# Performance work log

Hardware: AMD Instinct MI355X
Metric: run time of the kernel (lower is better)

## Reference

```python
import jax, jax.numpy as jnp
import numpy as np

H = 128  # lstm_hidden_dim


def setup_inputs() -> dict:
    key = jax.random.key(0)
    ks = jax.random.split(key, 7)
    T, B, D = 512, 1024, 128
    s = 1.0 / np.sqrt(H)  # pytorch default LSTM init scale
    return {
        "inp": jax.random.normal(ks[0], (T, B, D), dtype=jnp.float32),
        "W_ih": jax.random.uniform(ks[1], (4 * H, D), jnp.float32, -s, s),
        "W_hh": jax.random.uniform(ks[2], (4 * H, H), jnp.float32, -s, s),
        "b_ih": jax.random.uniform(ks[3], (4 * H,), jnp.float32, -s, s),
        "b_hh": jax.random.uniform(ks[4], (4 * H,), jnp.float32, -s, s),
        "W_lin": jax.random.uniform(ks[5], (H, H), jnp.float32, -s, s),
        "b_lin": jax.random.uniform(ks[6], (H,), jnp.float32, -s, s),
        "future": 128,
    }


def _lstm_cell(x, h, c, W_ih, W_hh, b_ih, b_hh):
    # gates: [B, 4H], PyTorch gate order i, f, g, o
    gates = x @ W_ih.T + b_ih + h @ W_hh.T + b_hh
    i, f, g, o = jnp.split(gates, 4, axis=-1)
    i, f, o = jax.nn.sigmoid(i), jax.nn.sigmoid(f), jax.nn.sigmoid(o)
    g = jnp.tanh(g)
    c_new = f * c + i * g
    h_new = o * jnp.tanh(c_new)
    return h_new, c_new


def reference(inp, W_ih, W_hh, b_ih, b_hh, W_lin, b_lin, future):
    B = inp.shape[1]
    h0 = jnp.zeros((B, H), inp.dtype)
    c0 = jnp.zeros((B, H), inp.dtype)

    def scan_step(carry, x):
        h, c = carry
        h, c = _lstm_cell(x, h, c, W_ih, W_hh, b_ih, b_hh)
        return (h, c), None

    (h, c), _ = jax.lax.scan(scan_step, (h0, c0), inp)
    out = h @ W_lin.T + b_lin  # [B, H]

    def fut_step(carry, _):
        o, h, c = carry
        h, c = _lstm_cell(o, h, c, W_ih, W_hh, b_ih, b_hh)
        o = h @ W_lin.T + b_lin
        return (o, h, c), o

    (_, _, _), fut_outs = jax.lax.scan(fut_step, (out, h, c), None, length=future)
    # outputs: [future + 1, B, H]
    return jnp.concatenate([out[None], fut_outs], axis=0)
```

## Files before the change

### kernel.cpp

```cpp
#include <hip/hip_runtime.h>

#define TSTEPS 512
#define BATCH  1024
#define DIM    128
#define HID    128
#define FUT    128
#define BTILE  4
#define NBLOCKS (BATCH / BTILE)
#define NTHREADS 512
#define LSTR   136

typedef __bf16 bf16x8 __attribute__((ext_vector_type(8)));
typedef float  f32x4  __attribute__((ext_vector_type(4)));
typedef unsigned int uint32x2 __attribute__((ext_vector_type(2)));

#define LOG2E 1.4426950408889634f

#if defined(__has_builtin)
#if __has_builtin(__builtin_amdgcn_permlane16_swap) && __has_builtin(__builtin_amdgcn_permlane32_swap)
#define HAVE_PERMSWAP 1
#endif
#endif
#ifndef HAVE_PERMSWAP
#define HAVE_PERMSWAP 0
#endif

__device__ __forceinline__ bf16x8 ldfrag(const float* __restrict__ p) {
    f32x4 a = *(const f32x4*)p;
    f32x4 b = *(const f32x4*)(p + 4);
    bf16x8 r;
    r[0] = (__bf16)a[0]; r[1] = (__bf16)a[1]; r[2] = (__bf16)a[2]; r[3] = (__bf16)a[3];
    r[4] = (__bf16)b[0]; r[5] = (__bf16)b[1]; r[6] = (__bf16)b[2]; r[7] = (__bf16)b[3];
    return r;
}

__device__ __forceinline__ float cell_update(f32x4 gv, float& c) {
    float pi = gv[0], pf = gv[1], pg = gv[2], po = gv[3];
    float ti = __builtin_amdgcn_exp2f(-LOG2E        * __builtin_fabsf(pi));
    float tf = __builtin_amdgcn_exp2f(-LOG2E        * __builtin_fabsf(pf));
    float tg = __builtin_amdgcn_exp2f(-2.0f * LOG2E * __builtin_fabsf(pg));
    float to = __builtin_amdgcn_exp2f(-LOG2E        * __builtin_fabsf(po));
    float di = 1.0f + ti, df = 1.0f + tf, dg = 1.0f + tg, dox = 1.0f + to;
    float p1 = di * df, p2 = dg * dox;
    float invP  = __builtin_amdgcn_rcpf(p1 * p2);
    float inv12 = invP * p2;
    float inv34 = invP * p1;
    float ig = ((pi >= 0.0f) ? 1.0f : ti) * (inv12 * df);
    float fg = ((pf >= 0.0f) ? 1.0f : tf) * (inv12 * di);
    float og = ((po >= 0.0f) ? 1.0f : to) * (inv34 * dg);
    float gg = __builtin_copysignf((1.0f - tg) * (inv34 * dox), pg);
    c = fg * c + ig * gg;
    float tc  = __builtin_amdgcn_exp2f(-2.0f * LOG2E * __builtin_fabsf(c));
    float thc = __builtin_copysignf((1.0f - tc) * __builtin_amdgcn_rcpf(1.0f + tc), c);
    return og * thc;
}

__device__ __forceinline__ float sel4(int q, float b0, float b1, float b2, float b3) {
    float lo = (q & 1) ? b1 : b0;
    float hi = (q & 1) ? b3 : b2;
    return (q & 2) ? hi : lo;
}

#if HAVE_PERMSWAP
__device__ __forceinline__ float gate_gather_perm(f32x4 a, bool r1_16, bool r1_32) {
    uint32x2 s01 = __builtin_amdgcn_permlane16_swap(__float_as_uint(a[0]), __float_as_uint(a[1]), false, false);
    uint32x2 s23 = __builtin_amdgcn_permlane16_swap(__float_as_uint(a[2]), __float_as_uint(a[3]), false, false);
    unsigned lo = r1_16 ? s01[1] : s01[0];
    unsigned hi = r1_16 ? s23[1] : s23[0];
    uint32x2 fin = __builtin_amdgcn_permlane32_swap(lo, hi, false, false);
    return __uint_as_float(r1_32 ? fin[1] : fin[0]);
}
#endif

__global__ __launch_bounds__(NTHREADS, 2)
void lstm_forecast(const float* __restrict__ inp,
                   const float* __restrict__ W_ih, const float* __restrict__ W_hh,
                   const float* __restrict__ b_ih, const float* __restrict__ b_hh,
                   const float* __restrict__ W_lin, const float* __restrict__ b_lin,
                   float* __restrict__ out)
{
    __shared__ __bf16 x_sh[2][16 * LSTR];
    __shared__ __bf16 h_sh[2][16 * LSTR];

    const int tid  = threadIdx.x;
    const int lane = tid & 63;
    const int wave = tid >> 6;
    const int q    = lane >> 4;
    const int m    = lane & 15;
    const int bo   = blockIdx.x * BTILE;

    for (int i = tid; i < 16 * LSTR; i += NTHREADS) {
        x_sh[0][i] = (__bf16)0.0f;
        x_sh[1][i] = (__bf16)0.0f;
        h_sh[0][i] = (__bf16)0.0f;
        h_sh[1][i] = (__bf16)0.0f;
    }

    bool use_perm = false, r1_16 = false, r1_32 = false;
    int  fmap = 0;
#if HAVE_PERMSWAP
    {
        unsigned lid = (unsigned)lane;
        uint32x2 t16 = __builtin_amdgcn_permlane16_swap(lid, lid + 1000u, false, false);
        unsigned v16 = (unsigned)__builtin_amdgcn_readlane((int)t16[0], 0);
        uint32x2 t32 = __builtin_amdgcn_permlane32_swap(lid, lid + 1000u, false, false);
        unsigned v32 = (unsigned)__builtin_amdgcn_readlane((int)t32[0], 0);
        bool ok16 = (v16 == 0u) || (v16 == 16u) || (v16 == 1000u) || (v16 == 1016u);
        bool ok32 = (v32 == 0u) || (v32 == 32u) || (v32 == 1000u) || (v32 == 1032u);
        r1_16 = (v16 == 16u) || (v16 == 1016u);
        r1_32 = (v32 == 32u) || (v32 == 1032u);
        bool fl16 = (v16 >= 1000u);
        bool fl32 = (v32 >= 1000u);
        use_perm = ok16 && ok32;
        fmap = (fl16 ? 1 : 0) | (fl32 ? 2 : 0);
    }
#endif

    bf16x8 wih[4][4], whh[4][4], wlin[4];
    float  bias_g[4];
    #pragma unroll
    for (int g = 0; g < 4; ++g) {
        const int n = g * HID + wave * 16 + m;
        bias_g[g] = b_ih[n] + b_hh[n];
        #pragma unroll
        for (int kt = 0; kt < 4; ++kt) {
            wih[g][kt] = ldfrag(W_ih + (size_t)n * DIM + kt * 32 + q * 8);
            whh[g][kt] = ldfrag(W_hh + (size_t)n * HID + kt * 32 + q * 8);
        }
    }
    const int   nl     = wave * 16 + m;
    const float bias_l = b_lin[nl];
    #pragma unroll
    for (int kt = 0; kt < 4; ++kt)
        wlin[kt] = ldfrag(W_lin + (size_t)nl * HID + kt * 32 + q * 8);

    const int rb = use_perm ? (q ^ fmap) : q;
    const int jj = wave * 16 + m;
    float creg = 0.0f;

    const int lk    = m * LSTR + q * 8;
    const int paddr = (lane & 15) << 2;

    const int cr = tid >> 7, cc = tid & 127;
    const float* xptr = inp + (size_t)(bo + cr) * DIM + cc;
    const size_t XS = (size_t)BATCH * DIM;
    const int xrowb = 4 * (use_perm ? (cr ^ fmap) : cr);

    float bank0[8], bank1[8];
    #pragma unroll
    for (int k = 0; k < 8; ++k) {
        bank0[k] = xptr[(size_t)k * XS];
        bank1[k] = xptr[(size_t)(8 + k) * XS];
    }

    __syncthreads();

    f32x4 xacc[4];

    for (int tb = 0; tb < TSTEPS; tb += 16) {
        #pragma unroll
        for (int j = 0; j < 16; ++j) {
            const int p = j & 1;
            if ((j & 3) == 0) {
                #pragma unroll
                for (int k = 0; k < 4; ++k) {
                    float xv = ((j + k) < 8) ? bank0[j + k] : bank1[j + k - 8];
                    x_sh[0][(xrowb + k) * LSTR + cc] = (__bf16)xv;
                }
            }
            __syncthreads();

            if (j == 7) {
                if (tb + 16 < TSTEPS) {
                    #pragma unroll
                    for (int k = 0; k < 8; ++k)
                        bank0[k] = xptr[(size_t)(tb + 16 + k) * XS];
                }
            }
            if (j == 15) {
                if (tb + 24 < TSTEPS) {
                    #pragma unroll
                    for (int k = 0; k < 8; ++k)
                        bank1[k] = xptr[(size_t)(tb + 24 + k) * XS];
                }
            }

            if ((j & 3) == 0) {
                #pragma unroll
                for (int g = 0; g < 4; ++g)
                    xacc[g] = (f32x4){bias_g[g], bias_g[g], bias_g[g], bias_g[g]};
                #pragma unroll
                for (int kt = 0; kt < 4; ++kt) {
                    bf16x8 ax = *(const bf16x8*)&x_sh[0][lk + kt * 32];
                    #pragma unroll
                    for (int g = 0; g < 4; ++g)
                        xacc[g] = __builtin_amdgcn_mfma_f32_16x16x32_bf16(ax, wih[g][kt], xacc[g], 0, 0, 0);
                }
            }

            f32x4 hacc[4];
            #pragma unroll
            for (int g = 0; g < 4; ++g)
                hacc[g] = (f32x4){0.0f, 0.0f, 0.0f, 0.0f};
            #pragma unroll
            for (int kt = 0; kt < 4; ++kt) {
                bf16x8 ah = *(const bf16x8*)&h_sh[p][lk + kt * 32];
                #pragma unroll
                for (int g = 0; g < 4; ++g)
                    hacc[g] = __builtin_amdgcn_mfma_f32_16x16x32_bf16(ah, whh[g][kt], hacc[g], 0, 0, 0);
            }

            f32x4 gv;
#if HAVE_PERMSWAP
            if (use_perm) {
                #pragma unroll
                for (int g = 0; g < 4; ++g)
                    gv[g] = gate_gather_perm(hacc[g], r1_16, r1_32) + xacc[g][j & 3];
            } else
#endif
            {
                #pragma unroll
                for (int g = 0; g < 4; ++g) {
                    float b0 = __int_as_float(__builtin_amdgcn_ds_bpermute(paddr, __float_as_int(hacc[g][0])));
                    float b1 = __int_as_float(__builtin_amdgcn_ds_bpermute(paddr, __float_as_int(hacc[g][1])));
                    float b2 = __int_as_float(__builtin_amdgcn_ds_bpermute(paddr, __float_as_int(hacc[g][2])));
                    float b3 = __int_as_float(__builtin_amdgcn_ds_bpermute(paddr, __float_as_int(hacc[g][3])));
                    gv[g] = sel4(q, b0, b1, b2, b3) + xacc[g][j & 3];
                }
            }

            float h = cell_update(gv, creg);
            h_sh[p ^ 1][rb * LSTR + jj] = (__bf16)h;
        }
    }

    for (int i = tid; i < 16 * LSTR; i += NTHREADS)
        if (i >= 4 * LSTR) x_sh[0][i] = (__bf16)0.0f;

    int ph = 0;
    for (int tf = 0; tf <= FUT; ++tf) {
        __syncthreads();
        f32x4 accl = (f32x4){bias_l, bias_l, bias_l, bias_l};
        #pragma unroll
        for (int kt = 0; kt < 4; ++kt) {
            bf16x8 ah = *(const bf16x8*)&h_sh[ph][lk + kt * 32];
            accl = __builtin_amdgcn_mfma_f32_16x16x32_bf16(ah, wlin[kt], accl, 0, 0, 0);
        }
        if (q == 0) {
            #pragma unroll
            for (int r = 0; r < 4; ++r) {
                float o = accl[r];
                out[(size_t)tf * BATCH * HID + (size_t)(bo + r) * HID + nl] = o;
                if (tf < FUT) {
                    __bf16 hi = (__bf16)o;
                    x_sh[0][r * LSTR + nl] = hi;
                    x_sh[1][r * LSTR + nl] = (__bf16)(o - (float)hi);
                }
            }
        }
        if (tf == FUT) break;
        __syncthreads();

        f32x4 acc[4];
        #pragma unroll
        for (int g = 0; g < 4; ++g)
            acc[g] = (f32x4){bias_g[g], bias_g[g], bias_g[g], bias_g[g]};
        #pragma unroll
        for (int kt = 0; kt < 4; ++kt) {
            bf16x8 axh = *(const bf16x8*)&x_sh[0][lk + kt * 32];
            bf16x8 axl = *(const bf16x8*)&x_sh[1][lk + kt * 32];
            bf16x8 ah  = *(const bf16x8*)&h_sh[ph][lk + kt * 32];
            #pragma unroll
            for (int g = 0; g < 4; ++g) {
                acc[g] = __builtin_amdgcn_mfma_f32_16x16x32_bf16(axh, wih[g][kt], acc[g], 0, 0, 0);
                acc[g] = __builtin_amdgcn_mfma_f32_16x16x32_bf16(axl, wih[g][kt], acc[g], 0, 0, 0);
                acc[g] = __builtin_amdgcn_mfma_f32_16x16x32_bf16(ah,  whh[g][kt], acc[g], 0, 0, 0);
            }
        }
        f32x4 gv;
#if HAVE_PERMSWAP
        if (use_perm) {
            #pragma unroll
            for (int g = 0; g < 4; ++g)
                gv[g] = gate_gather_perm(acc[g], r1_16, r1_32);
        } else
#endif
        {
            #pragma unroll
            for (int g = 0; g < 4; ++g) {
                float b0 = __int_as_float(__builtin_amdgcn_ds_bpermute(paddr, __float_as_int(acc[g][0])));
                float b1 = __int_as_float(__builtin_amdgcn_ds_bpermute(paddr, __float_as_int(acc[g][1])));
                float b2 = __int_as_float(__builtin_amdgcn_ds_bpermute(paddr, __float_as_int(acc[g][2])));
                float b3 = __int_as_float(__builtin_amdgcn_ds_bpermute(paddr, __float_as_int(acc[g][3])));
                gv[g] = sel4(q, b0, b1, b2, b3);
            }
        }

        float h = cell_update(gv, creg);
        h_sh[ph ^ 1][rb * LSTR + jj] = (__bf16)h;
        ph ^= 1;
    }
}

extern "C" void kernel_launch(void* const* d_in, const int* in_sizes, int n_in,
                              void* d_out, int out_size, void* d_ws, size_t ws_size,
                              hipStream_t stream) {
    const float* inp   = (const float*)d_in[0];
    const float* W_ih  = (const float*)d_in[1];
    const float* W_hh  = (const float*)d_in[2];
    const float* b_ih  = (const float*)d_in[3];
    const float* b_hh  = (const float*)d_in[4];
    const float* W_lin = (const float*)d_in[5];
    const float* b_lin = (const float*)d_in[6];
    float* out = (float*)d_out;

    hipLaunchKernelGGL(lstm_forecast, dim3(NBLOCKS), dim3(NTHREADS), 0, stream,
                       inp, W_ih, W_hh, b_ih, b_hh, W_lin, b_lin, out);
}
```

Measured before the change: 845.3 us.

## Fold linear projection into future-step LSTM weights via precomputed fused matrix

Adds a prep kernel that computes W_fut = W_hh + W_ih·W_lin and a fused bias (b_ih + b_hh + W_ih·b_lin), so each future step needs one 128-wide matmul on h instead of separate x (hi/lo split) and h matmuls plus an extra barrier. It also masks h fragment loads to the 4 valid batch rows so LDS reads for padding rows are skipped. The fused weight is rounded to bf16, which drops the hi/lo precision split on the output feedback and may add error over 128 recurrent steps. It also costs one extra kernel launch and a global weight read per block.

```diff
diff --git a/kernel.cpp b/kernel.cpp
--- a/kernel.cpp
+++ b/kernel.cpp
@@ -25,12 +25,22 @@
 #define HAVE_PERMSWAP 0
 #endif
 
+__device__ __bf16 g_wfut[4 * HID * HID];
+__device__ float  g_wfutb[4 * HID];
+
 __device__ __forceinline__ bf16x8 ldfrag(const float* __restrict__ p) {
     f32x4 a = *(const f32x4*)p;
     f32x4 b = *(const f32x4*)(p + 4);
     bf16x8 r;
     r[0] = (__bf16)a[0]; r[1] = (__bf16)a[1]; r[2] = (__bf16)a[2]; r[3] = (__bf16)a[3];
     r[4] = (__bf16)b[0]; r[5] = (__bf16)b[1]; r[6] = (__bf16)b[2]; r[7] = (__bf16)b[3];
+    return r;
+}
+
+__device__ __forceinline__ bf16x8 zfrag() {
+    bf16x8 r;
+    #pragma unroll
+    for (int i = 0; i < 8; ++i) r[i] = (__bf16)0.0f;
     return r;
 }
 
@@ -72,6 +82,39 @@
 }
 #endif
 
+__global__ __launch_bounds__(512)
+void prep_wfut(const float* __restrict__ W_ih, const float* __restrict__ W_hh,
+               const float* __restrict__ b_ih, const float* __restrict__ b_hh,
+               const float* __restrict__ W_lin, const float* __restrict__ b_lin)
+{
+    __shared__ float wl[64 * 128];
+    __shared__ float sc[512];
+    const int tid = threadIdx.x;
+    const int r = tid >> 7, k = tid & 127;
+    const int n = blockIdx.x * 4 + r;
+
+    float acc = W_hh[(size_t)n * HID + k];
+    #pragma unroll
+    for (int half = 0; half < 2; ++half) {
+        __syncthreads();
+        for (int i = tid; i < 64 * 128; i += 512)
+            wl[i] = W_lin[half * 64 * 128 + i];
+        __syncthreads();
+        #pragma unroll 8
+        for (int d = 0; d < 64; ++d)
+            acc += W_ih[(size_t)n * DIM + half * 64 + d] * wl[d * 128 + k];
+    }
+    g_wfut[(size_t)n * HID + k] = (__bf16)acc;
+
+    sc[tid] = W_ih[(size_t)n * DIM + k] * b_lin[k];
+    __syncthreads();
+    for (int s = 64; s > 0; s >>= 1) {
+        if (k < s) sc[r * 128 + k] += sc[r * 128 + k + s];
+        __syncthreads();
+    }
+    if (k == 0) g_wfutb[n] = b_ih[n] + b_hh[n] + sc[r * 128];
+}
+
 __global__ __launch_bounds__(NTHREADS, 2)
 void lstm_forecast(const float* __restrict__ inp,
                    const float* __restrict__ W_ih, const float* __restrict__ W_hh,
@@ -79,7 +122,7 @@
                    const float* __restrict__ W_lin, const float* __restrict__ b_lin,
                    float* __restrict__ out)
 {
-    __shared__ __bf16 x_sh[2][16 * LSTR];
+    __shared__ __bf16 x_sh[16 * LSTR];
     __shared__ __bf16 h_sh[2][16 * LSTR];
 
     const int tid  = threadIdx.x;
@@ -90,8 +133,7 @@
     const int bo   = blockIdx.x * BTILE;
 
     for (int i = tid; i < 16 * LSTR; i += NTHREADS) {
-        x_sh[0][i] = (__bf16)0.0f;
-        x_sh[1][i] = (__bf16)0.0f;
+        x_sh[i] = (__bf16)0.0f;
         h_sh[0][i] = (__bf16)0.0f;
         h_sh[1][i] = (__bf16)0.0f;
     }
@@ -165,7 +207,7 @@
                 #pragma unroll
                 for (int k = 0; k < 4; ++k) {
                     float xv = ((j + k) < 8) ? bank0[j + k] : bank1[j + k - 8];
-                    x_sh[0][(xrowb + k) * LSTR + cc] = (__bf16)xv;
+                    x_sh[(xrowb + k) * LSTR + cc] = (__bf16)xv;
                 }
             }
             __syncthreads();
@@ -191,7 +233,7 @@
                     xacc[g] = (f32x4){bias_g[g], bias_g[g], bias_g[g], bias_g[g]};
                 #pragma unroll
                 for (int kt = 0; kt < 4; ++kt) {
-                    bf16x8 ax = *(const bf16x8*)&x_sh[0][lk + kt * 32];
+                    bf16x8 ax = *(const bf16x8*)&x_sh[lk + kt * 32];
                     #pragma unroll
                     for (int g = 0; g < 4; ++g)
                         xacc[g] = __builtin_amdgcn_mfma_f32_16x16x32_bf16(ax, wih[g][kt], xacc[g], 0, 0, 0);
@@ -204,7 +246,8 @@
                 hacc[g] = (f32x4){0.0f, 0.0f, 0.0f, 0.0f};
             #pragma unroll
             for (int kt = 0; kt < 4; ++kt) {
-                bf16x8 ah = *(const bf16x8*)&h_sh[p][lk + kt * 32];
+                bf16x8 ah = zfrag();
+                if (m < BTILE) ah = *(const bf16x8*)&h_sh[p][lk + kt * 32];
                 #pragma unroll
                 for (int g = 0; g < 4; ++g)
                     hacc[g] = __builtin_amdgcn_mfma_f32_16x16x32_bf16(ah, whh[g][kt], hacc[g], 0, 0, 0);
@@ -234,64 +277,64 @@
         }
     }
 
-    for (int i = tid; i < 16 * LSTR; i += NTHREADS)
-        if (i >= 4 * LSTR) x_sh[0][i] = (__bf16)0.0f;
+    bf16x8 wfut[4][4];
+    float  bias_f[4];
+    #pragma unroll
+    for (int g = 0; g < 4; ++g) {
+        const int n = g * HID + nl;
+        bias_f[g] = g_wfutb[n];
+        #pragma unroll
+        for (int kt = 0; kt < 4; ++kt)
+            wfut[g][kt] = *(const bf16x8*)(g_wfut + (size_t)n * HID + kt * 32 + q * 8);
+    }
 
     int ph = 0;
     for (int tf = 0; tf <= FUT; ++tf) {
         __syncthreads();
+        bf16x8 ahf[4];
+        #pragma unroll
+        for (int kt = 0; kt < 4; ++kt) {
+            ahf[kt] = zfrag();
+            if (m < BTILE) ahf[kt] = *(const bf16x8*)&h_sh[ph][lk + kt * 32];
+        }
+
         f32x4 accl = (f32x4){bias_l, bias_l, bias_l, bias_l};
         #pragma unroll
+        for (int kt = 0; kt < 4; ++kt)
+            accl = __builtin_amdgcn_mfma_f32_16x16x32_bf16(ahf[kt], wlin[kt], accl, 0, 0, 0);
+        if (q == 0) {
+            #pragma unroll
+            for (int r = 0; r < 4; ++r)
+                out[(size_t)tf * BATCH * HID + (size_t)(bo + r) * HID + nl] = accl[r];
+        }
+        if (tf == FUT) break;
+
+        f32x4 facc[4];
+        #pragma unroll
+        for (int g = 0; g < 4; ++g)
+            facc[g] = (f32x4){bias_f[g], bias_f[g], bias_f[g], bias_f[g]};
+        #pragma unroll
         for (int kt = 0; kt < 4; ++kt) {
-            bf16x8 ah = *(const bf16x8*)&h_sh[ph][lk + kt * 32];
-            accl = __builtin_amdgcn_mfma_f32_16x16x32_bf16(ah, wlin[kt], accl, 0, 0, 0);
-        }
-        if (q == 0) {
-            #pragma unroll
-            for (int r = 0; r < 4; ++r) {
-                float o = accl[r];
-                out[(size_t)tf * BATCH * HID + (size_t)(bo + r) * HID + nl] = o;
-                if (tf < FUT) {
-                    __bf16 hi = (__bf16)o;
-                    x_sh[0][r * LSTR + nl] = hi;
-                    x_sh[1][r * LSTR + nl] = (__bf16)(o - (float)hi);
-                }
-            }
-        }
-        if (tf == FUT) break;
-        __syncthreads();
-
-        f32x4 acc[4];
-        #pragma unroll
-        for (int g = 0; g < 4; ++g)
-            acc[g] = (f32x4){bias_g[g], bias_g[g], bias_g[g], bias_g[g]};
-        #pragma unroll
-        for (int kt = 0; kt < 4; ++kt) {
-            bf16x8 axh = *(const bf16x8*)&x_sh[0][lk + kt * 32];
-            bf16x8 axl = *(const bf16x8*)&x_sh[1][lk + kt * 32];
-            bf16x8 ah  = *(const bf16x8*)&h_sh[ph][lk + kt * 32];
-            #pragma unroll
-            for (int g = 0; g < 4; ++g) {
-                acc[g] = __builtin_amdgcn_mfma_f32_16x16x32_bf16(axh, wih[g][kt], acc[g], 0, 0, 0);
-                acc[g] = __builtin_amdgcn_mfma_f32_16x16x32_bf16(axl, wih[g][kt], acc[g], 0, 0, 0);
-                acc[g] = __builtin_amdgcn_mfma_f32_16x16x32_bf16(ah,  whh[g][kt], acc[g], 0, 0, 0);
-            }
-        }
+            #pragma unroll
+            for (int g = 0; g < 4; ++g)
+                facc[g] = __builtin_amdgcn_mfma_f32_16x16x32_bf16(ahf[kt], wfut[g][kt], facc[g], 0, 0, 0);
+        }
+
         f32x4 gv;
 #if HAVE_PERMSWAP
         if (use_perm) {
             #pragma unroll
             for (int g = 0; g < 4; ++g)
-                gv[g] = gate_gather_perm(acc[g], r1_16, r1_32);
+                gv[g] = gate_gather_perm(facc[g], r1_16, r1_32);
         } else
 #endif
         {
             #pragma unroll
             for (int g = 0; g < 4; ++g) {
-                float b0 = __int_as_float(__builtin_amdgcn_ds_bpermute(paddr, __float_as_int(acc[g][0])));
-                float b1 = __int_as_float(__builtin_amdgcn_ds_bpermute(paddr, __float_as_int(acc[g][1])));
-                float b2 = __int_as_float(__builtin_amdgcn_ds_bpermute(paddr, __float_as_int(acc[g][2])));
-                float b3 = __int_as_float(__builtin_amdgcn_ds_bpermute(paddr, __float_as_int(acc[g][3])));
+                float b0 = __int_as_float(__builtin_amdgcn_ds_bpermute(paddr, __float_as_int(facc[g][0])));
+                float b1 = __int_as_float(__builtin_amdgcn_ds_bpermute(paddr, __float_as_int(facc[g][1])));
+                float b2 = __int_as_float(__builtin_amdgcn_ds_bpermute(paddr, __float_as_int(facc[g][2])));
+                float b3 = __int_as_float(__builtin_amdgcn_ds_bpermute(paddr, __float_as_int(facc[g][3])));
                 gv[g] = sel4(q, b0, b1, b2, b3);
             }
         }
@@ -314,6 +357,8 @@
     const float* b_lin = (const float*)d_in[6];
     float* out = (float*)d_out;
 
+    hipLaunchKernelGGL(prep_wfut, dim3(128), dim3(512), 0, stream,
+                       W_ih, W_hh, b_ih, b_hh, W_lin, b_lin);
     hipLaunchKernelGGL(lstm_forecast, dim3(NBLOCKS), dim3(NTHREADS), 0, stream,
                        inp, W_ih, W_hh, b_ih, b_hh, W_lin, b_lin, out);
 }
```

Measured after the change: 810.6 us. 1.04x faster.
